# Performance work log

Measured on AMD Instinct MI355X. Metric: run time of the kernel, lower is better.

The kernel has to match this reference:

```python
import jax, jax.numpy as jnp
from jax import lax
import numpy as np

B, K, H, W = 16, 8, 256, 256


def setup_inputs() -> dict:
    key = jax.random.key(0)
    masks = jax.random.normal(key, (B, K, H, W), dtype=jnp.float32)
    return {"masks": masks}


def _nlccs_loss_one(mask):
    """Per-mask loss. mask: (H, W) float, already rescaled/clamped.

    Replicates cv2.connectedComponentsWithStats (8-connectivity, background is
    a single label regardless of connectivity), sorts components by area, and
    suppresses (zeroes a pmask over) the bounding box of the second-largest
    component, then returns mean(pmask * mask).
    """
    h, w = mask.shape
    S = h * w  # sentinel / background label
    sent = jnp.int32(S)
    fg = lax.stop_gradient(mask) > 0.5  # cv2 threshold (arr > 0.5)
    idx = jnp.arange(S, dtype=jnp.int32).reshape(h, w)
    lab0 = jnp.where(fg, idx, sent)

    def step(lab):
        # 8-connectivity neighbor-min propagation (cv2 default connectivity=8)
        p = jnp.pad(lab, 1, constant_values=S)
        m = lab
        for dy in (-1, 0, 1):
            for dx in (-1, 0, 1):
                if dy == 0 and dx == 0:
                    continue
                m = jnp.minimum(m, p[1 + dy:1 + dy + h, 1 + dx:1 + dx + w])
        lab = jnp.where(fg, m, sent)
        # pointer jumping: lab <- lab[lab] for log-time convergence
        ext = jnp.concatenate([lab.reshape(-1), jnp.array([S], jnp.int32)])
        return jnp.where(fg, ext[lab], sent)

    def cond(c):
        lab, prev = c
        return jnp.any(lab != prev)

    def body(c):
        lab, _ = c
        return step(lab), lab

    lab, _ = lax.while_loop(cond, body, (step(lab0), lab0))

    # per-label areas; background pixels all share label S (like cv2 label 0)
    areas = jnp.zeros(S + 1, jnp.int32).at[lab.reshape(-1)].add(1)
    _, top_idx = lax.top_k(areas, 2)
    second = top_idx[1]  # stats sorted by area -> stats[-2]

    # bounding box of the second-largest component
    sel = lab == second
    rows = jnp.arange(h, dtype=jnp.int32)[:, None]
    cols = jnp.arange(w, dtype=jnp.int32)[None, :]
    h0 = jnp.min(jnp.where(sel, rows, h))
    h1 = jnp.max(jnp.where(sel, rows, -1)) + 1
    w0 = jnp.min(jnp.where(sel, cols, w))
    w1 = jnp.max(jnp.where(sel, cols, -1)) + 1
    inside = (rows >= h0) & (rows < h1) & (cols >= w0) & (cols < w1)
    pmask = 1.0 - inside.astype(mask.dtype)  # pmask[h0:h1, w0:w1] = 0
    return (pmask * mask).mean()


def reference(masks):
    # masks: (b, k, h, w)
    m = jnp.maximum((masks + 1.0) * 0.5, 0.0)  # ((masks+1)/2).clamp(min=0)
    flat = m.reshape(-1, m.shape[-2], m.shape[-1])  # (b*k, h, w)
    losses = jax.vmap(_nlccs_loss_one)(flat)
    return losses.mean()
```

## Files before the change

### kernel.cpp

```cpp
#include <hip/hip_runtime.h>

#define HH 256
#define WW 256
#define SS 65536
#define NM 128
#define TRR 16
#define NT2 16
#define RMX 2048
#define SPT 1024
#define SPM 16384

struct Meta {
  double dsum[NM];
  int h0[NM]; int h1[NM]; int w0[NM]; int w1[NM];
};

__device__ __forceinline__ int find_c(int* L, int x) {
  int p = L[x];
  if (p == x) return x;
  int root = p, q = L[root];
  while (q != root) { root = q; q = L[root]; }
  if (root != p) L[x] = root;
  return root;
}

__device__ __forceinline__ void unite(int* L, int a, int b) {
  bool done = false;
  do {
    a = find_c(L, a);
    b = find_c(L, b);
    if (a < b)      { int old = atomicMin(&L[b], a); done = (old == b); b = old; }
    else if (b < a) { int old = atomicMin(&L[a], b); done = (old == a); a = old; }
    else done = true;
  } while (!done);
}

__device__ __forceinline__ int find_halve(int* L, int x) {
  int p = L[x];
  while (p != x) {
    int gp = L[p];
    if (gp == p) return p;
    L[x] = gp;
    x = p; p = gp;
  }
  return x;
}

__device__ __forceinline__ int cid(const unsigned long long* rm,
                                   const int* rpre, int r) {
  int w = r >> 6, b = r & 63;
  return rpre[w] + (int)__popcll(rm[w] & (b ? ((1ull << b) - 1) : 0ull));
}

__device__ __forceinline__ unsigned long long mask_le(int b) {
  return (b == 63) ? ~0ull : ((1ull << (b + 1)) - 1);
}
__device__ __forceinline__ unsigned long long mask_lt(int b) {
  return b ? ((1ull << b) - 1) : 0ull;
}

__global__ __launch_bounds__(512)
void k_local(const float* __restrict__ in, int cb,
             int* __restrict__ gp, int* __restrict__ ga,
             unsigned int* __restrict__ gbb, unsigned short* __restrict__ gl,
             unsigned short* __restrict__ gbrow, int* __restrict__ gnr,
             double* __restrict__ tdsum, unsigned int* __restrict__ tbb,
             int* __restrict__ gfg0) {
  __shared__ unsigned long long sfgw[TRR][4];
  __shared__ unsigned char sfgc[TRR][32];
  __shared__ unsigned long long srs[TRR][4];
  __shared__ int wpre64[64];
  __shared__ int snr;
  __shared__ int sspan[RMX];
  __shared__ int suf[RMX];
  __shared__ unsigned long long rootm[32];
  __shared__ int rpre[32];
  __shared__ int sA[SPT], sW0[SPT], sW1[SPT], sH0[SPT], sH1[SPT];
  __shared__ double sred[8];
  __shared__ int sbb[4][8];

  int q = blockIdx.x, lm = q >> 4, tile = q & 15;
  int tid = threadIdx.x, lane = tid & 63, wv = tid >> 6;
  int gm = cb + lm, R0 = tile << 4;

  int r1 = tid >> 5, cs = tid & 31;
  const float4* src =
      (const float4*)(in + ((size_t)gm << 16) + ((R0 + r1) << 8) + (cs << 3));
  double dsum = 0.0;
  unsigned int fgb = 0;
  for (int k = 0; k < 2; k++) {
    float4 v = src[k];
    float m0 = fmaxf((v.x + 1.0f) * 0.5f, 0.0f);
    float m1 = fmaxf((v.y + 1.0f) * 0.5f, 0.0f);
    float m2 = fmaxf((v.z + 1.0f) * 0.5f, 0.0f);
    float m3 = fmaxf((v.w + 1.0f) * 0.5f, 0.0f);
    dsum += (double)m0 + (double)m1 + (double)m2 + (double)m3;
    fgb |= ((m0 > 0.5f) ? 1u : 0u) << (4 * k);
    fgb |= ((m1 > 0.5f) ? 1u : 0u) << (4 * k + 1);
    fgb |= ((m2 > 0.5f) ? 1u : 0u) << (4 * k + 2);
    fgb |= ((m3 > 0.5f) ? 1u : 0u) << (4 * k + 3);
  }
  sfgc[r1][cs] = (unsigned char)fgb;
  __syncthreads();
  if (tid < 64) {
    int row = tid >> 2, w = tid & 3;
    const unsigned char* pc = &sfgc[row][w << 3];
    unsigned long long wd = 0;
    for (int i = 0; i < 8; i++) wd |= ((unsigned long long)pc[i]) << (i << 3);
    sfgw[row][w] = wd;
  }
  __syncthreads();

  if (tid < 64) {
    int row = tid >> 2, w = tid & 3;
    unsigned long long W = sfgw[row][w];
    unsigned long long carry = (w > 0) ? (sfgw[row][w - 1] >> 63) : 0ull;
    unsigned long long rs = W & ~((W << 1) | carry);
    srs[row][w] = rs;
    int cnt = (int)__popcll(rs);
    int sa = cnt;
    for (int off = 1; off < 64; off <<= 1) {
      int t = __shfl_up(sa, off);
      if (tid >= off) sa += t;
    }
    wpre64[tid] = sa - cnt;
    if (tid == 63) snr = sa;
    int id = sa - cnt;
    unsigned long long bits = rs;
    while (bits) {
      int a = (int)__ffsll(bits) - 1;
      bits &= bits - 1;
      int A = (w << 6) + a;
      unsigned long long inv = ~(W >> a);
      int len = inv ? ((int)__ffsll(inv) - 1) : (64 - a);
      if (len == 64 - a) {
        for (int w2 = w + 1; w2 < 4; w2++) {
          unsigned long long iv2 = ~sfgw[row][w2];
          int t = iv2 ? ((int)__ffsll(iv2) - 1) : 64;
          len += t;
          if (t < 64) break;
        }
      }
      sspan[id] = (row << 16) | (A << 8) | (A + len - 1);
      suf[id] = id;
      id++;
    }
  } else {
    for (int s = tid - 64; s < SPT; s += 448) {
      sA[s] = 0; sW0[s] = WW; sW1[s] = -1; sH0[s] = TRR; sH1[s] = -1;
    }
  }
  __syncthreads();

  int nr = snr;

  for (int i = tid; i < nr; i += 512) {
    int sp = sspan[i];
    int row = sp >> 16, a = (sp >> 8) & 255, b = sp & 255;
    if (row == 0) continue;
    int lo = max(a - 1, 0), hi = min(b + 1, 255);
    const unsigned long long* Wp = sfgw[row - 1];
    const unsigned long long* Rp = srs[row - 1];
    int prebase = (row - 1) << 2;
    int lw = lo >> 6, lb = lo & 63;
    if (((Wp[lw] >> lb) & 1) && !((Rp[lw] >> lb) & 1)) {
      int j = wpre64[prebase + lw] + (int)__popcll(Rp[lw] & mask_le(lb)) - 1;
      unite(suf, i, j);
    }
    for (int w = lw; w <= (hi >> 6); w++) {
      unsigned long long m = Rp[w];
      if (w == lw) m &= ~mask_lt(lb);
      if (w == (hi >> 6)) m &= mask_le(hi & 63);
      int base2 = wpre64[prebase + w];
      while (m) {
        int bb = (int)__ffsll(m) - 1;
        m &= m - 1;
        int j = base2 + (int)__popcll(Rp[w] & mask_lt(bb));
        unite(suf, i, j);
      }
    }
  }
  __syncthreads();

  for (int j = 0; j < 4; j++) {
    int i = tid + (j << 9);
    unsigned long long bal = __ballot(i < nr && suf[i] == i);
    if (lane == 0) rootm[wv + (j << 3)] = bal;
  }
  __syncthreads();
  if (tid < 32) {
    int pc = (int)__popcll(rootm[tid]);
    int sa = pc;
    for (int off = 1; off < 32; off <<= 1) {
      int t = __shfl_up(sa, off);
      if (tid >= off) sa += t;
    }
    rpre[tid] = sa - pc;
  }
  __syncthreads();

  for (int i = tid; i < nr; i += 512) {
    int root = find_halve(suf, i);
    int id = cid(rootm, rpre, root);
    int sp = sspan[i];
    int row = sp >> 16, a = (sp >> 8) & 255, b = sp & 255;
    atomicAdd(&sA[id], b - a + 1);
    if (a < sW0[id]) atomicMin(&sW0[id], a);
    if (b > sW1[id]) atomicMax(&sW1[id], b);
    if (row < sH0[id]) atomicMin(&sH0[id], row);
    if (row > sH1[id]) atomicMax(&sH1[id], row);
  }
  __syncthreads();

  int nc = rpre[31] + (int)__popcll(rootm[31]);
  for (int i = tid; i < nr; i += 512) {
    if (suf[i] == i) {
      int id = cid(rootm, rpre, i);
      int gid = (lm << 14) + (tile << 10) + id;
      int sp = sspan[i];
      gp[gid] = gid;
      ga[gid] = sA[id];
      gl[gid] = (unsigned short)((tile << 12) + ((sp >> 16) << 8) +
                                 ((sp >> 8) & 255));
      gbb[gid] = ((unsigned)(R0 + sH0[id]) << 24) | ((unsigned)sW0[id] << 16)
               | ((unsigned)(R0 + sH1[id]) << 8) | (unsigned)sW1[id];
    }
  }
  {
    int c = tid & 255, topbot = tid >> 8;
    int brow = topbot ? (TRR - 1) : 0;
    unsigned short val = 0xFFFF;
    if ((sfgw[brow][c >> 6] >> (c & 63)) & 1) {
      int w = c >> 6, bb = c & 63;
      int id = wpre64[(brow << 2) + w] +
               (int)__popcll(srs[brow][w] & mask_le(bb)) - 1;
      int root = find_halve(suf, id);
      val = (unsigned short)((tile << 10) + cid(rootm, rpre, root));
    }
    gbrow[(q << 9) + (topbot ? 256 : 0) + c] = val;
  }
  if (tid == 0) gnr[q] = nc;

  int c = tid & 255, half = (tid >> 8) << 3;
  int bh0r = TRR, bh1r = -1;
  bool anybg = false;
  for (int row = half; row < half + 8; row++) {
    if (!((sfgw[row][c >> 6] >> (c & 63)) & 1)) {
      anybg = true;
      bh0r = min(bh0r, row); bh1r = max(bh1r, row);
    }
  }
  int bw0r = anybg ? c : WW, bw1r = anybg ? c : -1;
  for (int off = 32; off > 0; off >>= 1) {
    bw0r = min(bw0r, __shfl_down(bw0r, off));
    bw1r = max(bw1r, __shfl_down(bw1r, off));
    bh0r = min(bh0r, __shfl_down(bh0r, off));
    bh1r = max(bh1r, __shfl_down(bh1r, off));
  }
  if (lane == 0) { sbb[0][wv] = bw0r; sbb[1][wv] = bw1r;
                   sbb[2][wv] = bh0r; sbb[3][wv] = bh1r; }
  for (int off = 32; off > 0; off >>= 1) dsum += __shfl_down(dsum, off);
  if (lane == 0) sred[wv] = dsum;
  __syncthreads();
  if (tid == 0) {
    int a0 = sbb[0][0], a1 = sbb[1][0], a2 = sbb[2][0], a3 = sbb[3][0];
    for (int i = 1; i < 8; i++) {
      a0 = min(a0, sbb[0][i]); a1 = max(a1, sbb[1][i]);
      a2 = min(a2, sbb[2][i]); a3 = max(a3, sbb[3][i]);
    }
    unsigned pack = (a1 >= 0)
        ? (((unsigned)(R0 + a2) << 24) | ((unsigned)a0 << 16) |
           ((unsigned)(R0 + a3) << 8) | (unsigned)a1)
        : 0xFFFF0000u;
    tbb[q] = pack;
    double t = 0.0;
    for (int i = 0; i < 8; i++) t += sred[i];
    tdsum[q] = t;
    if (tile == 0) gfg0[lm] = (int)(sfgw[0][0] & 1ull);
  }
}

__global__ __launch_bounds__(512)
void k_tail(int c0,
            const int* __restrict__ ga,
            const unsigned int* __restrict__ gbb,
            const unsigned short* __restrict__ gl,
            const unsigned short* __restrict__ gbrow,
            const int* __restrict__ gnr,
            const double* __restrict__ tdsum,
            const unsigned int* __restrict__ tbb,
            const int* __restrict__ gfg0,
            Meta* __restrict__ mt) {
  __shared__ int par[SPM];
  __shared__ int sar[SPM];
  __shared__ int pre[17];
  __shared__ int snc[16];
  __shared__ unsigned long long stt1[16], stt2[16];
  __shared__ int stfs[16];
  __shared__ int ssel;
  __shared__ int sbr[4][8];

  int lm = blockIdx.x, gm = c0 + lm;
  int tid = threadIdx.x, lane = tid & 63, wv = tid >> 6;
  int tb = lm << 4, sbase = lm << 14;

  if (tid < 16) snc[tid] = gnr[tb + tid];
  __syncthreads();
  if (tid == 0) {
    int s = 0;
    for (int t = 0; t < 16; t++) { pre[t] = s; s += snc[t]; }
    pre[16] = s;
  }
  __syncthreads();
  int ncm = pre[16];

  for (int t = 0; t < 16; t++) {
    int nc = snc[t], base = pre[t], gbase = sbase + (t << 10);
    for (int sl = tid; sl < nc; sl += 512) {
      par[base + sl] = base + sl;
      sar[base + sl] = ga[gbase + sl];
    }
  }
  __syncthreads();

  for (int idx = tid; idx < 15 * 256; idx += 512) {
    int s = idx >> 8, c = idx & 255;
    const unsigned short* up = gbrow + ((tb + s) << 9) + 256;
    const unsigned short* lo = gbrow + ((tb + s + 1) << 9);
    unsigned short v16 = lo[c];
    if (v16 == 0xFFFF) continue;
    int v = pre[v16 >> 10] + (v16 & 1023);
    bool wfg = (c > 0) && (lo[c - 1] != 0xFFFF);
    unsigned short n16 = up[c];
    if (!wfg) {
      if (n16 != 0xFFFF) unite(par, v, pre[n16 >> 10] + (n16 & 1023));
      else if (c > 0 && up[c - 1] != 0xFFFF) {
        unsigned short o = up[c - 1];
        unite(par, v, pre[o >> 10] + (o & 1023));
      }
    }
    if (n16 == 0xFFFF && c < 255 && up[c + 1] != 0xFFFF) {
      unsigned short o = up[c + 1];
      unite(par, v, pre[o >> 10] + (o & 1023));
    }
  }
  __syncthreads();

  for (int i = tid; i < ncm; i += 512) {
    int r = find_c(par, i);
    if (r != i) atomicAdd(&sar[r], sar[i]);
  }
  __syncthreads();

  for (int tt = 0; tt < 2; tt++) {
    int tile = (wv << 1) + tt;
    int nc = snc[tile], base = pre[tile], gbase = sbase + (tile << 10);
    unsigned long long t1 = 0, t2 = 0;
    int fsum = 0;
    for (int sl = lane; sl < nc; sl += 64) {
      int i = base + sl;
      if (par[i] == i) {
        int a = sar[i];
        int lab = gl[gbase + sl];
        fsum += a;
        unsigned long long key = ((unsigned long long)a << 37)
                               | ((unsigned long long)(SS - lab) << 20)
                               | (unsigned)((tile << 10) + sl);
        if (key > t1) { t2 = t1; t1 = key; }
        else if (key > t2) t2 = key;
      }
    }
    for (int off = 32; off > 0; off >>= 1) {
      unsigned long long o1 = __shfl_down(t1, off), o2 = __shfl_down(t2, off);
      if (o1 > t1) { t2 = (t1 > o2) ? t1 : o2; t1 = o1; }
      else if (o1 > t2) t2 = o1;
      fsum += __shfl_down(fsum, off);
    }
    if (lane == 0) { stt1[tile] = t1; stt2[tile] = t2; stfs[tile] = fsum; }
  }
  __syncthreads();

  if (tid < 64) {
    double d = 0.0;
    int h0 = 255, w0 = 255, h1 = 0, w1 = 0;
    unsigned long long t1 = 0, t2 = 0;
    int fsum = 0;
    if (tid < 16) {
      d = tdsum[tb + tid];
      unsigned bb = tbb[tb + tid];
      h0 = (int)(bb >> 24); w0 = (int)((bb >> 16) & 255);
      h1 = (int)((bb >> 8) & 255); w1 = (int)(bb & 255);
      t1 = stt1[tid]; t2 = stt2[tid]; fsum = stfs[tid];
    }
    for (int off = 8; off > 0; off >>= 1) {
      d += __shfl_down(d, off);
      h0 = min(h0, __shfl_down(h0, off));
      w0 = min(w0, __shfl_down(w0, off));
      h1 = max(h1, __shfl_down(h1, off));
      w1 = max(w1, __shfl_down(w1, off));
      unsigned long long o1 = __shfl_down(t1, off), o2 = __shfl_down(t2, off);
      if (o1 > t1) { t2 = (t1 > o2) ? t1 : o2; t1 = o1; }
      else if (o1 > t2) t2 = o1;
      fsum += __shfl_down(fsum, off);
    }
    if (tid == 0) {
      mt->dsum[gm] = d;
      unsigned long long bg = ((unsigned long long)(SS - fsum)) << 37;
      int zl = gfg0[lm] ? 1 : 0;
      unsigned long long zk = ((unsigned long long)(SS - zl)) << 20;
      if (bg > t1) { t2 = t1; t1 = bg; } else if (bg > t2) t2 = bg;
      if (zk > t1) { t2 = t1; t1 = zk; } else if (zk > t2) t2 = zk;
      if (t2 == bg) {
        mt->h0[gm] = h0; mt->h1[gm] = h1; mt->w0[gm] = w0; mt->w1[gm] = w1;
        ssel = -1;
      } else if (t2 == zk) {
        mt->h0[gm] = 1; mt->h1[gm] = 0; mt->w0[gm] = 1; mt->w1[gm] = 0;
        ssel = -1;
      } else {
        int s = (int)(t2 & 0xFFFFF);
        ssel = pre[s >> 10] + (s & 1023);
      }
    }
  }
  __syncthreads();

  int rsel = ssel;
  if (rsel >= 0) {
    int bh0 = HH, bw0 = WW, bh1 = -1, bw1 = -1;
    for (int t = 0; t < 16; t++) {
      int nc = snc[t], base = pre[t], gbase = sbase + (t << 10);
      for (int sl = tid; sl < nc; sl += 512) {
        int i = base + sl;
        if (par[i] == rsel) {
          unsigned int bb = gbb[gbase + sl];
          bh0 = min(bh0, (int)(bb >> 24));
          bw0 = min(bw0, (int)((bb >> 16) & 255));
          bh1 = max(bh1, (int)((bb >> 8) & 255));
          bw1 = max(bw1, (int)(bb & 255));
        }
      }
    }
    for (int off = 32; off > 0; off >>= 1) {
      bh0 = min(bh0, __shfl_down(bh0, off));
      bw0 = min(bw0, __shfl_down(bw0, off));
      bh1 = max(bh1, __shfl_down(bh1, off));
      bw1 = max(bw1, __shfl_down(bw1, off));
    }
    if (lane == 0) { sbr[0][wv] = bh0; sbr[1][wv] = bw0;
                     sbr[2][wv] = bh1; sbr[3][wv] = bw1; }
    __syncthreads();
    if (tid == 0) {
      int a0 = sbr[0][0], a1 = sbr[1][0], a2 = sbr[2][0], a3 = sbr[3][0];
      for (int i = 1; i < 8; i++) {
        a0 = min(a0, sbr[0][i]); a1 = min(a1, sbr[1][i]);
        a2 = max(a2, sbr[2][i]); a3 = max(a3, sbr[3][i]);
      }
      mt->h0[gm] = a0; mt->w0[gm] = a1; mt->h1[gm] = a2; mt->w1[gm] = a3;
    }
  }
}

__global__ void k_inside(const float* __restrict__ in,
                         const Meta* __restrict__ mt,
                         double* __restrict__ dinsp, int c0) {
  int b = blockIdx.x;
  int lm = b >> 3, seg = b & 7;
  int gm = c0 + lm;
  int h0 = mt->h0[gm], h1 = mt->h1[gm], w0 = mt->w0[gm], w1 = mt->w1[gm];
  double acc = 0.0;
  if (h1 >= h0) {
    int cc = w0 + threadIdx.x;
    if (cc <= w1) {
      const float* base = in + ((size_t)gm << 16);
      for (int rr = h0 + seg; rr <= h1; rr += 8) {
        float x = base[(rr << 8) + cc];
        acc += (double)fmaxf((x + 1.0f) * 0.5f, 0.0f);
      }
    }
  }
  for (int off = 32; off > 0; off >>= 1) acc += __shfl_down(acc, off);
  __shared__ double sd[4];
  int wid = threadIdx.x >> 6, lane = threadIdx.x & 63;
  if (lane == 0) sd[wid] = acc;
  __syncthreads();
  if (threadIdx.x == 0)
    dinsp[(gm << 3) + seg] = sd[0] + sd[1] + sd[2] + sd[3];
}

__global__ void k_final(const Meta* __restrict__ mt,
                        const double* __restrict__ dinsp,
                        float* __restrict__ out) {
  __shared__ double sd[NM];
  int t = threadIdx.x;
  double di = 0.0;
  for (int s = 0; s < 8; s++) di += dinsp[(t << 3) + s];
  sd[t] = (mt->dsum[t] - di) / (double)SS;
  __syncthreads();
  for (int off = 64; off > 0; off >>= 1) {
    if (t < off) sd[t] += sd[t + off];
    __syncthreads();
  }
  if (t == 0) out[0] = (float)(sd[0] / (double)NM);
}

extern "C" void kernel_launch(void* const* d_in, const int* in_sizes, int n_in,
                              void* d_out, int out_size, void* d_ws,
                              size_t ws_size, hipStream_t stream) {
  const float* in = (const float*)d_in[0];
  float* out = (float*)d_out;

  Meta* mt = (Meta*)d_ws;
  const size_t meta_bytes = (sizeof(Meta) + 255) & ~(size_t)255;
  char* base = (char*)d_ws + meta_bytes;
  size_t fixed = (size_t)NM * 8 * sizeof(double);
  size_t avail = (ws_size > meta_bytes + fixed)
                     ? (ws_size - meta_bytes - fixed) : 0;
  const size_t per_mask = (size_t)NT2 * 8 +
                          (size_t)SPM * (4 + 4 + 4 + 2) +
                          (size_t)NT2 * 512 * 2 +
                          (size_t)NT2 * 4 +
                          (size_t)NT2 * 4 +
                          4;
  int chunk = (int)(avail / per_mask);
  if (chunk > NM) chunk = NM;
  if (chunk < 1) return;

  char* ptr = base;
  double* dinsp = (double*)ptr;        ptr += fixed;
  double* tdsum = (double*)ptr;        ptr += (size_t)chunk * NT2 * 8;
  int* gp = (int*)ptr;                 ptr += (size_t)chunk * SPM * 4;
  int* ga = (int*)ptr;                 ptr += (size_t)chunk * SPM * 4;
  unsigned int* gbb = (unsigned int*)ptr;       ptr += (size_t)chunk * SPM * 4;
  unsigned short* gl = (unsigned short*)ptr;    ptr += (size_t)chunk * SPM * 2;
  unsigned short* gbrow = (unsigned short*)ptr; ptr += (size_t)chunk * NT2 * 512 * 2;
  int* gnr = (int*)ptr;                ptr += (size_t)chunk * NT2 * 4;
  unsigned int* tbb = (unsigned int*)ptr;       ptr += (size_t)chunk * NT2 * 4;
  int* gfg0 = (int*)ptr;

  for (int c0 = 0; c0 < NM; c0 += chunk) {
    int cn = (chunk < NM - c0) ? chunk : (NM - c0);
    k_local<<<cn * NT2, 512, 0, stream>>>(in, c0, gp, ga, gbb, gl, gbrow,
                                          gnr, tdsum, tbb, gfg0);
    k_tail <<<cn, 512, 0, stream>>>(c0, ga, gbb, gl, gbrow, gnr,
                                    tdsum, tbb, gfg0, mt);
    k_inside<<<cn * 8, 256, 0, stream>>>(in, mt, dinsp, c0);
  }
  k_final<<<1, 128, 0, stream>>>(mt, dinsp, out);
}
```

Before: 181.7 us.

## Fuse inside-box sum into tail kernel and drop compacted label indexing

Folds the k_inside bounding-box summation into k_tail, so each mask's block sums the suppressed region itself and writes a per-mask loss. This removes one kernel launch and the Meta round-trip through global memory. It also drops the unused gp array and the per-tile prefix compaction, addressing union-find slots directly as tile*1024+id. In exchange k_tail now initializes and scans the full 16384 slots instead of only the live components, and the box sum runs on one block per mask rather than eight.

```diff
diff --git a/kernel.cpp b/kernel.cpp
--- a/kernel.cpp
+++ b/kernel.cpp
@@ -10,11 +10,6 @@
 #define SPT 1024
 #define SPM 16384
 
-struct Meta {
-  double dsum[NM];
-  int h0[NM]; int h1[NM]; int w0[NM]; int w1[NM];
-};
-
 __device__ __forceinline__ int find_c(int* L, int x) {
   int p = L[x];
   if (p == x) return x;
@@ -61,7 +56,7 @@
 
 __global__ __launch_bounds__(512)
 void k_local(const float* __restrict__ in, int cb,
-             int* __restrict__ gp, int* __restrict__ ga,
+             int* __restrict__ ga,
              unsigned int* __restrict__ gbb, unsigned short* __restrict__ gl,
              unsigned short* __restrict__ gbrow, int* __restrict__ gnr,
              double* __restrict__ tdsum, unsigned int* __restrict__ tbb,
@@ -218,7 +213,6 @@
       int id = cid(rootm, rpre, i);
       int gid = (lm << 14) + (tile << 10) + id;
       int sp = sspan[i];
-      gp[gid] = gid;
       ga[gid] = sA[id];
       gl[gid] = (unsigned short)((tile << 12) + ((sp >> 16) << 8) +
                                  ((sp >> 8) & 255));
@@ -281,7 +275,7 @@
 }
 
 __global__ __launch_bounds__(512)
-void k_tail(int c0,
+void k_tail(const float* __restrict__ in, int c0,
             const int* __restrict__ ga,
             const unsigned int* __restrict__ gbb,
             const unsigned short* __restrict__ gl,
@@ -290,15 +284,18 @@
             const double* __restrict__ tdsum,
             const unsigned int* __restrict__ tbb,
             const int* __restrict__ gfg0,
-            Meta* __restrict__ mt) {
+            double* __restrict__ lossv) {
   __shared__ int par[SPM];
   __shared__ int sar[SPM];
-  __shared__ int pre[17];
   __shared__ int snc[16];
   __shared__ unsigned long long stt1[16], stt2[16];
   __shared__ int stfs[16];
   __shared__ int ssel;
+  __shared__ int sbx[4];
   __shared__ int sbr[4][8];
+  __shared__ double sdl[2][4];
+  __shared__ double dseg[8];
+  __shared__ double sdsum;
 
   int lm = blockIdx.x, gm = c0 + lm;
   int tid = threadIdx.x, lane = tid & 63, wv = tid >> 6;
@@ -306,20 +303,11 @@
 
   if (tid < 16) snc[tid] = gnr[tb + tid];
   __syncthreads();
-  if (tid == 0) {
-    int s = 0;
-    for (int t = 0; t < 16; t++) { pre[t] = s; s += snc[t]; }
-    pre[16] = s;
-  }
-  __syncthreads();
-  int ncm = pre[16];
-
-  for (int t = 0; t < 16; t++) {
-    int nc = snc[t], base = pre[t], gbase = sbase + (t << 10);
-    for (int sl = tid; sl < nc; sl += 512) {
-      par[base + sl] = base + sl;
-      sar[base + sl] = ga[gbase + sl];
-    }
+
+  for (int idx = tid; idx < SPM; idx += 512) {
+    par[idx] = idx;
+    int sl = idx & 1023, t = idx >> 10;
+    sar[idx] = (sl < snc[t]) ? ga[sbase + idx] : 0;
   }
   __syncthreads();
 
@@ -329,24 +317,19 @@
     const unsigned short* lo = gbrow + ((tb + s + 1) << 9);
     unsigned short v16 = lo[c];
     if (v16 == 0xFFFF) continue;
-    int v = pre[v16 >> 10] + (v16 & 1023);
+    int v = v16;
     bool wfg = (c > 0) && (lo[c - 1] != 0xFFFF);
     unsigned short n16 = up[c];
     if (!wfg) {
-      if (n16 != 0xFFFF) unite(par, v, pre[n16 >> 10] + (n16 & 1023));
-      else if (c > 0 && up[c - 1] != 0xFFFF) {
-        unsigned short o = up[c - 1];
-        unite(par, v, pre[o >> 10] + (o & 1023));
-      }
-    }
-    if (n16 == 0xFFFF && c < 255 && up[c + 1] != 0xFFFF) {
-      unsigned short o = up[c + 1];
-      unite(par, v, pre[o >> 10] + (o & 1023));
-    }
-  }
-  __syncthreads();
-
-  for (int i = tid; i < ncm; i += 512) {
+      if (n16 != 0xFFFF) unite(par, v, (int)n16);
+      else if (c > 0 && up[c - 1] != 0xFFFF) unite(par, v, (int)up[c - 1]);
+    }
+    if (n16 == 0xFFFF && c < 255 && up[c + 1] != 0xFFFF)
+      unite(par, v, (int)up[c + 1]);
+  }
+  __syncthreads();
+
+  for (int i = tid; i < SPM; i += 512) {
     int r = find_c(par, i);
     if (r != i) atomicAdd(&sar[r], sar[i]);
   }
@@ -354,18 +337,18 @@
 
   for (int tt = 0; tt < 2; tt++) {
     int tile = (wv << 1) + tt;
-    int nc = snc[tile], base = pre[tile], gbase = sbase + (tile << 10);
+    int nc = snc[tile], base = tile << 10;
     unsigned long long t1 = 0, t2 = 0;
     int fsum = 0;
     for (int sl = lane; sl < nc; sl += 64) {
       int i = base + sl;
       if (par[i] == i) {
         int a = sar[i];
-        int lab = gl[gbase + sl];
+        int lab = gl[sbase + i];
         fsum += a;
         unsigned long long key = ((unsigned long long)a << 37)
                                | ((unsigned long long)(SS - lab) << 20)
-                               | (unsigned)((tile << 10) + sl);
+                               | (unsigned)i;
         if (key > t1) { t2 = t1; t1 = key; }
         else if (key > t2) t2 = key;
       }
@@ -404,21 +387,20 @@
       fsum += __shfl_down(fsum, off);
     }
     if (tid == 0) {
-      mt->dsum[gm] = d;
+      sdsum = d;
       unsigned long long bg = ((unsigned long long)(SS - fsum)) << 37;
       int zl = gfg0[lm] ? 1 : 0;
       unsigned long long zk = ((unsigned long long)(SS - zl)) << 20;
       if (bg > t1) { t2 = t1; t1 = bg; } else if (bg > t2) t2 = bg;
       if (zk > t1) { t2 = t1; t1 = zk; } else if (zk > t2) t2 = zk;
       if (t2 == bg) {
-        mt->h0[gm] = h0; mt->h1[gm] = h1; mt->w0[gm] = w0; mt->w1[gm] = w1;
+        sbx[0] = h0; sbx[1] = h1; sbx[2] = w0; sbx[3] = w1;
         ssel = -1;
       } else if (t2 == zk) {
-        mt->h0[gm] = 1; mt->h1[gm] = 0; mt->w0[gm] = 1; mt->w1[gm] = 0;
+        sbx[0] = 1; sbx[1] = 0; sbx[2] = 1; sbx[3] = 0;
         ssel = -1;
       } else {
-        int s = (int)(t2 & 0xFFFFF);
-        ssel = pre[s >> 10] + (s & 1023);
+        ssel = (int)(t2 & 0xFFFFF);
       }
     }
   }
@@ -427,17 +409,13 @@
   int rsel = ssel;
   if (rsel >= 0) {
     int bh0 = HH, bw0 = WW, bh1 = -1, bw1 = -1;
-    for (int t = 0; t < 16; t++) {
-      int nc = snc[t], base = pre[t], gbase = sbase + (t << 10);
-      for (int sl = tid; sl < nc; sl += 512) {
-        int i = base + sl;
-        if (par[i] == rsel) {
-          unsigned int bb = gbb[gbase + sl];
-          bh0 = min(bh0, (int)(bb >> 24));
-          bw0 = min(bw0, (int)((bb >> 16) & 255));
-          bh1 = max(bh1, (int)((bb >> 8) & 255));
-          bw1 = max(bw1, (int)(bb & 255));
-        }
+    for (int idx = tid; idx < SPM; idx += 512) {
+      if (par[idx] == rsel) {
+        unsigned int bb = gbb[sbase + idx];
+        bh0 = min(bh0, (int)(bb >> 24));
+        bw0 = min(bw0, (int)((bb >> 16) & 255));
+        bh1 = max(bh1, (int)((bb >> 8) & 255));
+        bw1 = max(bw1, (int)(bb & 255));
       }
     }
     for (int off = 32; off > 0; off >>= 1) {
@@ -455,46 +433,48 @@
         a0 = min(a0, sbr[0][i]); a1 = min(a1, sbr[1][i]);
         a2 = max(a2, sbr[2][i]); a3 = max(a3, sbr[3][i]);
       }
-      mt->h0[gm] = a0; mt->w0[gm] = a1; mt->h1[gm] = a2; mt->w1[gm] = a3;
-    }
-  }
-}
-
-__global__ void k_inside(const float* __restrict__ in,
-                         const Meta* __restrict__ mt,
-                         double* __restrict__ dinsp, int c0) {
-  int b = blockIdx.x;
-  int lm = b >> 3, seg = b & 7;
-  int gm = c0 + lm;
-  int h0 = mt->h0[gm], h1 = mt->h1[gm], w0 = mt->w0[gm], w1 = mt->w1[gm];
-  double acc = 0.0;
-  if (h1 >= h0) {
-    int cc = w0 + threadIdx.x;
-    if (cc <= w1) {
-      const float* base = in + ((size_t)gm << 16);
-      for (int rr = h0 + seg; rr <= h1; rr += 8) {
-        float x = base[(rr << 8) + cc];
-        acc += (double)fmaxf((x + 1.0f) * 0.5f, 0.0f);
-      }
-    }
-  }
-  for (int off = 32; off > 0; off >>= 1) acc += __shfl_down(acc, off);
-  __shared__ double sd[4];
-  int wid = threadIdx.x >> 6, lane = threadIdx.x & 63;
-  if (lane == 0) sd[wid] = acc;
-  __syncthreads();
-  if (threadIdx.x == 0)
-    dinsp[(gm << 3) + seg] = sd[0] + sd[1] + sd[2] + sd[3];
-}
-
-__global__ void k_final(const Meta* __restrict__ mt,
-                        const double* __restrict__ dinsp,
+      sbx[0] = a0; sbx[2] = a1; sbx[1] = a2; sbx[3] = a3;
+    }
+  }
+  __syncthreads();
+
+  int h0 = sbx[0], h1 = sbx[1], w0 = sbx[2], w1 = sbx[3];
+  for (int r = 0; r < 4; r++) {
+    int g = tid >> 8;
+    int seg = (r << 1) + g;
+    int t256 = tid & 255;
+    double acc = 0.0;
+    if (h1 >= h0) {
+      int cc = w0 + t256;
+      if (cc <= w1) {
+        const float* base = in + ((size_t)gm << 16);
+        for (int rr = h0 + seg; rr <= h1; rr += 8) {
+          float x = base[(rr << 8) + cc];
+          acc += (double)fmaxf((x + 1.0f) * 0.5f, 0.0f);
+        }
+      }
+    }
+    for (int off = 32; off > 0; off >>= 1) acc += __shfl_down(acc, off);
+    if (lane == 0) sdl[g][t256 >> 6] = acc;
+    __syncthreads();
+    if (tid == 0) {
+      dseg[(r << 1)] = sdl[0][0] + sdl[0][1] + sdl[0][2] + sdl[0][3];
+      dseg[(r << 1) + 1] = sdl[1][0] + sdl[1][1] + sdl[1][2] + sdl[1][3];
+    }
+    __syncthreads();
+  }
+  if (tid == 0) {
+    double di = 0.0;
+    for (int s = 0; s < 8; s++) di += dseg[s];
+    lossv[gm] = (sdsum - di) / (double)SS;
+  }
+}
+
+__global__ void k_final(const double* __restrict__ lossv,
                         float* __restrict__ out) {
   __shared__ double sd[NM];
   int t = threadIdx.x;
-  double di = 0.0;
-  for (int s = 0; s < 8; s++) di += dinsp[(t << 3) + s];
-  sd[t] = (mt->dsum[t] - di) / (double)SS;
+  sd[t] = lossv[t];
   __syncthreads();
   for (int off = 64; off > 0; off >>= 1) {
     if (t < off) sd[t] += sd[t + off];
@@ -509,14 +489,12 @@
   const float* in = (const float*)d_in[0];
   float* out = (float*)d_out;
 
-  Meta* mt = (Meta*)d_ws;
-  const size_t meta_bytes = (sizeof(Meta) + 255) & ~(size_t)255;
-  char* base = (char*)d_ws + meta_bytes;
-  size_t fixed = (size_t)NM * 8 * sizeof(double);
-  size_t avail = (ws_size > meta_bytes + fixed)
-                     ? (ws_size - meta_bytes - fixed) : 0;
+  double* lossv = (double*)d_ws;
+  const size_t loss_bytes = (NM * sizeof(double) + 255) & ~(size_t)255;
+  char* base = (char*)d_ws + loss_bytes;
+  size_t avail = (ws_size > loss_bytes) ? (ws_size - loss_bytes) : 0;
   const size_t per_mask = (size_t)NT2 * 8 +
-                          (size_t)SPM * (4 + 4 + 4 + 2) +
+                          (size_t)SPM * (4 + 4 + 2) +
                           (size_t)NT2 * 512 * 2 +
                           (size_t)NT2 * 4 +
                           (size_t)NT2 * 4 +
@@ -526,9 +504,7 @@
   if (chunk < 1) return;
 
   char* ptr = base;
-  double* dinsp = (double*)ptr;        ptr += fixed;
   double* tdsum = (double*)ptr;        ptr += (size_t)chunk * NT2 * 8;
-  int* gp = (int*)ptr;                 ptr += (size_t)chunk * SPM * 4;
   int* ga = (int*)ptr;                 ptr += (size_t)chunk * SPM * 4;
   unsigned int* gbb = (unsigned int*)ptr;       ptr += (size_t)chunk * SPM * 4;
   unsigned short* gl = (unsigned short*)ptr;    ptr += (size_t)chunk * SPM * 2;
@@ -539,11 +515,10 @@
 
   for (int c0 = 0; c0 < NM; c0 += chunk) {
     int cn = (chunk < NM - c0) ? chunk : (NM - c0);
-    k_local<<<cn * NT2, 512, 0, stream>>>(in, c0, gp, ga, gbb, gl, gbrow,
+    k_local<<<cn * NT2, 512, 0, stream>>>(in, c0, ga, gbb, gl, gbrow,
                                           gnr, tdsum, tbb, gfg0);
-    k_tail <<<cn, 512, 0, stream>>>(c0, ga, gbb, gl, gbrow, gnr,
-                                    tdsum, tbb, gfg0, mt);
-    k_inside<<<cn * 8, 256, 0, stream>>>(in, mt, dinsp, c0);
-  }
-  k_final<<<1, 128, 0, stream>>>(mt, dinsp, out);
-}
+    k_tail <<<cn, 512, 0, stream>>>(in, c0, ga, gbb, gl, gbrow, gnr,
+                                    tdsum, tbb, gfg0, lossv);
+  }
+  k_final<<<1, 128, 0, stream>>>(lossv, out);
+}
```

New measurement: 207.9 us. 1.14x slower.

## Use sparse fixed-slot indexing in tail kernel and stage boundary rows in LDS

Applied to the files above, without the earlier changes.

The tail kernel drops the prefix-compacted component numbering and instead indexes union-find slots directly as tile*1024+slot, so the boundary labels can be used as parent indices without a prefix lookup. The boundary rows are copied into shared memory with vectorized loads before the merge pass, and the unused gp global array write is removed from the local kernel. The cost is that init, flatten and bbox scans now cover all 16384 slots per mask instead of only the live component count, and the ga read is gated per slot.

```diff
diff --git a/kernel.cpp b/kernel.cpp
--- a/kernel.cpp
+++ b/kernel.cpp
@@ -61,7 +61,7 @@
 
 __global__ __launch_bounds__(512)
 void k_local(const float* __restrict__ in, int cb,
-             int* __restrict__ gp, int* __restrict__ ga,
+             int* __restrict__ ga,
              unsigned int* __restrict__ gbb, unsigned short* __restrict__ gl,
              unsigned short* __restrict__ gbrow, int* __restrict__ gnr,
              double* __restrict__ tdsum, unsigned int* __restrict__ tbb,
@@ -218,7 +218,6 @@
       int id = cid(rootm, rpre, i);
       int gid = (lm << 14) + (tile << 10) + id;
       int sp = sspan[i];
-      gp[gid] = gid;
       ga[gid] = sA[id];
       gl[gid] = (unsigned short)((tile << 12) + ((sp >> 16) << 8) +
                                  ((sp >> 8) & 255));
@@ -293,7 +292,7 @@
             Meta* __restrict__ mt) {
   __shared__ int par[SPM];
   __shared__ int sar[SPM];
-  __shared__ int pre[17];
+  __shared__ unsigned short sbrow[15 * 512];
   __shared__ int snc[16];
   __shared__ unsigned long long stt1[16], stt2[16];
   __shared__ int stfs[16];
@@ -305,48 +304,40 @@
   int tb = lm << 4, sbase = lm << 14;
 
   if (tid < 16) snc[tid] = gnr[tb + tid];
-  __syncthreads();
-  if (tid == 0) {
-    int s = 0;
-    for (int t = 0; t < 16; t++) { pre[t] = s; s += snc[t]; }
-    pre[16] = s;
-  }
-  __syncthreads();
-  int ncm = pre[16];
-
-  for (int t = 0; t < 16; t++) {
-    int nc = snc[t], base = pre[t], gbase = sbase + (t << 10);
-    for (int sl = tid; sl < nc; sl += 512) {
-      par[base + sl] = base + sl;
-      sar[base + sl] = ga[gbase + sl];
-    }
+
+  {
+    const uint4* gsrc = (const uint4*)(gbrow + (tb << 9) + 256);
+    uint4* dst = (uint4*)sbrow;
+    for (int i = tid; i < 960; i += 512) dst[i] = gsrc[i];
+  }
+  __syncthreads();
+
+  for (int idx = tid; idx < SPM; idx += 512) {
+    par[idx] = idx;
+    int sl = idx & 1023, t = idx >> 10;
+    sar[idx] = (sl < snc[t]) ? ga[sbase + idx] : 0;
   }
   __syncthreads();
 
   for (int idx = tid; idx < 15 * 256; idx += 512) {
     int s = idx >> 8, c = idx & 255;
-    const unsigned short* up = gbrow + ((tb + s) << 9) + 256;
-    const unsigned short* lo = gbrow + ((tb + s + 1) << 9);
+    const unsigned short* up = &sbrow[s << 9];
+    const unsigned short* lo = &sbrow[(s << 9) + 256];
     unsigned short v16 = lo[c];
     if (v16 == 0xFFFF) continue;
-    int v = pre[v16 >> 10] + (v16 & 1023);
+    int v = v16;
     bool wfg = (c > 0) && (lo[c - 1] != 0xFFFF);
     unsigned short n16 = up[c];
     if (!wfg) {
-      if (n16 != 0xFFFF) unite(par, v, pre[n16 >> 10] + (n16 & 1023));
-      else if (c > 0 && up[c - 1] != 0xFFFF) {
-        unsigned short o = up[c - 1];
-        unite(par, v, pre[o >> 10] + (o & 1023));
-      }
-    }
-    if (n16 == 0xFFFF && c < 255 && up[c + 1] != 0xFFFF) {
-      unsigned short o = up[c + 1];
-      unite(par, v, pre[o >> 10] + (o & 1023));
-    }
-  }
-  __syncthreads();
-
-  for (int i = tid; i < ncm; i += 512) {
+      if (n16 != 0xFFFF) unite(par, v, (int)n16);
+      else if (c > 0 && up[c - 1] != 0xFFFF) unite(par, v, (int)up[c - 1]);
+    }
+    if (n16 == 0xFFFF && c < 255 && up[c + 1] != 0xFFFF)
+      unite(par, v, (int)up[c + 1]);
+  }
+  __syncthreads();
+
+  for (int i = tid; i < SPM; i += 512) {
     int r = find_c(par, i);
     if (r != i) atomicAdd(&sar[r], sar[i]);
   }
@@ -354,18 +345,18 @@
 
   for (int tt = 0; tt < 2; tt++) {
     int tile = (wv << 1) + tt;
-    int nc = snc[tile], base = pre[tile], gbase = sbase + (tile << 10);
+    int nc = snc[tile], base = tile << 10;
     unsigned long long t1 = 0, t2 = 0;
     int fsum = 0;
     for (int sl = lane; sl < nc; sl += 64) {
       int i = base + sl;
       if (par[i] == i) {
         int a = sar[i];
-        int lab = gl[gbase + sl];
+        int lab = gl[sbase + i];
         fsum += a;
         unsigned long long key = ((unsigned long long)a << 37)
                                | ((unsigned long long)(SS - lab) << 20)
-                               | (unsigned)((tile << 10) + sl);
+                               | (unsigned)i;
         if (key > t1) { t2 = t1; t1 = key; }
         else if (key > t2) t2 = key;
       }
@@ -417,8 +408,7 @@
         mt->h0[gm] = 1; mt->h1[gm] = 0; mt->w0[gm] = 1; mt->w1[gm] = 0;
         ssel = -1;
       } else {
-        int s = (int)(t2 & 0xFFFFF);
-        ssel = pre[s >> 10] + (s & 1023);
+        ssel = (int)(t2 & 0xFFFFF);
       }
     }
   }
@@ -427,17 +417,13 @@
   int rsel = ssel;
   if (rsel >= 0) {
     int bh0 = HH, bw0 = WW, bh1 = -1, bw1 = -1;
-    for (int t = 0; t < 16; t++) {
-      int nc = snc[t], base = pre[t], gbase = sbase + (t << 10);
-      for (int sl = tid; sl < nc; sl += 512) {
-        int i = base + sl;
-        if (par[i] == rsel) {
-          unsigned int bb = gbb[gbase + sl];
-          bh0 = min(bh0, (int)(bb >> 24));
-          bw0 = min(bw0, (int)((bb >> 16) & 255));
-          bh1 = max(bh1, (int)((bb >> 8) & 255));
-          bw1 = max(bw1, (int)(bb & 255));
-        }
+    for (int idx = tid; idx < SPM; idx += 512) {
+      if (par[idx] == rsel) {
+        unsigned int bb = gbb[sbase + idx];
+        bh0 = min(bh0, (int)(bb >> 24));
+        bw0 = min(bw0, (int)((bb >> 16) & 255));
+        bh1 = max(bh1, (int)((bb >> 8) & 255));
+        bw1 = max(bw1, (int)(bb & 255));
       }
     }
     for (int off = 32; off > 0; off >>= 1) {
@@ -516,7 +502,7 @@
   size_t avail = (ws_size > meta_bytes + fixed)
                      ? (ws_size - meta_bytes - fixed) : 0;
   const size_t per_mask = (size_t)NT2 * 8 +
-                          (size_t)SPM * (4 + 4 + 4 + 2) +
+                          (size_t)SPM * (4 + 4 + 2) +
                           (size_t)NT2 * 512 * 2 +
                           (size_t)NT2 * 4 +
                           (size_t)NT2 * 4 +
@@ -528,7 +514,6 @@
   char* ptr = base;
   double* dinsp = (double*)ptr;        ptr += fixed;
   double* tdsum = (double*)ptr;        ptr += (size_t)chunk * NT2 * 8;
-  int* gp = (int*)ptr;                 ptr += (size_t)chunk * SPM * 4;
   int* ga = (int*)ptr;                 ptr += (size_t)chunk * SPM * 4;
   unsigned int* gbb = (unsigned int*)ptr;       ptr += (size_t)chunk * SPM * 4;
   unsigned short* gl = (unsigned short*)ptr;    ptr += (size_t)chunk * SPM * 2;
@@ -539,7 +524,7 @@
 
   for (int c0 = 0; c0 < NM; c0 += chunk) {
     int cn = (chunk < NM - c0) ? chunk : (NM - c0);
-    k_local<<<cn * NT2, 512, 0, stream>>>(in, c0, gp, ga, gbb, gl, gbrow,
+    k_local<<<cn * NT2, 512, 0, stream>>>(in, c0, ga, gbb, gl, gbrow,
                                           gnr, tdsum, tbb, gfg0);
     k_tail <<<cn, 512, 0, stream>>>(c0, ga, gbb, gl, gbrow, gnr,
                                     tdsum, tbb, gfg0, mt);
```

New measurement: 180.2 us. No clear change (-0.9%).
